# Optimization experiments

Hardware: AMD Instinct MI355X
Metric: run time of the kernel (lower is better)

## Reference

```python
import jax, jax.numpy as jnp
import numpy as np

DN = ('NHWC', 'HWIO', 'NHWC')

def conv(x, w, stride=1):
    return jax.lax.conv_general_dilated(x, w, (stride, stride), 'SAME', dimension_numbers=DN)

def up2(x):
    return jnp.repeat(jnp.repeat(x, 2, axis=1), 2, axis=2)

def nms(boxes, scores, max_output=100, iou_thresh=0.5):
    # greedy sequential NMS, fixed trip count, padded outputs
    NEG = jnp.float32(-1e30)
    area = (boxes[:, 2] - boxes[:, 0]) * (boxes[:, 3] - boxes[:, 1])  # [N]
    def step(sw, _):
        idx = jnp.argmax(sw)
        s = sw[idx]
        b = boxes[idx]
        valid = s > NEG * 0.5
        y1 = jnp.maximum(b[0], boxes[:, 0]); x1 = jnp.maximum(b[1], boxes[:, 1])
        y2 = jnp.minimum(b[2], boxes[:, 2]); x2 = jnp.minimum(b[3], boxes[:, 3])
        inter = jnp.maximum(y2 - y1, 0.0) * jnp.maximum(x2 - x1, 0.0)
        barea = (b[2] - b[0]) * (b[3] - b[1])
        iou = inter / (barea + area - inter + 1e-9)
        sw = jnp.where(iou > iou_thresh, NEG, sw)  # suppress (includes self)
        out_b = jnp.where(valid, b, jnp.zeros(4, boxes.dtype))
        out_s = jnp.where(valid, s, jnp.float32(0.0))
        return sw, (out_b, out_s)
    _, (sel_boxes, sel_scores) = jax.lax.scan(step, scores, None, length=max_output)
    return sel_boxes, sel_scores

def setup_inputs() -> dict:
    key = jax.random.key(0)
    ks = jax.random.split(key, 16)
    def w(k, shape):
        fan_in = shape[0] * shape[1] * shape[2]
        return jax.random.normal(k, shape, jnp.float32) * jnp.sqrt(2.0 / fan_in)
    return {
        'inputs': jax.random.normal(ks[0], (1, 512, 512, 3), jnp.float32),
        # backbone (resnet50-style channel widths, strides 2/4/8/16/32)
        'w_stem': w(ks[1], (7, 7, 3, 64)),
        'w_c2': w(ks[2], (3, 3, 64, 256)),
        'w_c3': w(ks[3], (3, 3, 256, 512)),
        'w_c4': w(ks[4], (3, 3, 512, 1024)),
        'w_c5': w(ks[5], (3, 3, 1024, 2048)),
        # FPN laterals + output convs (channels=256)
        'l3': w(ks[6], (1, 1, 512, 256)),
        'l4': w(ks[7], (1, 1, 1024, 256)),
        'l5': w(ks[8], (1, 1, 2048, 256)),
        'o3': w(ks[9], (3, 3, 256, 256)),
        'o4': w(ks[10], (3, 3, 256, 256)),
        'o5': w(ks[11], (3, 3, 256, 256)),
        # RPN: shared 3x3 + obj head (num_anchors=1) + bbox head (4*num_anchors)
        'w_rpn': w(ks[12], (3, 3, 256, 256)),
        'w_obj': w(ks[13], (1, 1, 256, 1)),
        'w_box': w(ks[14], (1, 1, 256, 4)),
    }

def reference(inputs, w_stem, w_c2, w_c3, w_c4, w_c5, l3, l4, l5, o3, o4, o5, w_rpn, w_obj, w_box):
    relu = jax.nn.relu
    # backbone
    s = relu(conv(inputs, w_stem, 2))   # 256x256x64
    c2 = relu(conv(s, w_c2, 2))         # 128x128x256
    c3 = relu(conv(c2, w_c3, 2))        # 64x64x512
    c4 = relu(conv(c3, w_c4, 2))        # 32x32x1024
    c5 = relu(conv(c4, w_c5, 2))        # 16x16x2048
    # FPN
    p5 = conv(c5, l5)
    p4 = conv(c4, l4) + up2(p5)
    p3 = conv(c3, l3) + up2(p4)
    p3, p4, p5 = conv(p3, o3), conv(p4, o4), conv(p5, o5)
    # RPN over all levels (bbox deltas computed per original but unused downstream)
    obj_logits = []
    for p in (p3, p4, p5):
        t = relu(conv(p, w_rpn))
        obj_logits.append(conv(t, w_obj))
        _ = conv(t, w_box)
    obj = obj_logits[0]  # [B, h, w, A]
    B, h, w_, A = obj.shape
    scores = jax.nn.sigmoid(obj).reshape(B, -1)  # [B, h*w*A]
    # anchor grid (fixed 0.1-sized boxes), faithful to TF meshgrid default 'xy' indexing
    yy = jnp.linspace(0.0, 1.0, h)
    xx = jnp.linspace(0.0, 1.0, w_)
    Y, X = jnp.meshgrid(yy, xx)  # shape [w, h]
    boxes = jnp.stack([Y - 0.05, X - 0.05, Y + 0.05, X + 0.05], axis=-1)
    boxes = jnp.clip(boxes, 0.0, 1.0).reshape(-1, 4)  # [w*h, 4]
    sel_boxes, sel_scores = nms(boxes, scores[0], max_output=100, iou_thresh=0.5)
    return sel_boxes, sel_scores
```

## Files before the change

### kernel.cpp

```cpp
#include <hip/hip_runtime.h>
#include <hip/hip_bf16.h>

typedef float f4 __attribute__((ext_vector_type(4)));
typedef short s8v __attribute__((ext_vector_type(8)));
typedef unsigned short us4 __attribute__((ext_vector_type(4)));
typedef unsigned short us8 __attribute__((ext_vector_type(8)));

#define AP 40

__global__ __launch_bounds__(256) void stem_kernel(
    const float* __restrict__ in, const float* __restrict__ w,
    float* __restrict__ out)
{
  __shared__ float in_lds[37 * 37 * 3];
  __shared__ float w_lds[7 * 7 * 3 * 64];
  const int tid = threadIdx.x;
  const int ty0 = (blockIdx.x >> 4) * 16;
  const int tx0 = (blockIdx.x & 15) * 16;

  for (int idx = tid; idx < 9408; idx += 256) w_lds[idx] = w[idx];
  for (int idx = tid; idx < 4107; idx += 256) {
    int ci = idx % 3;
    int rem = idx / 3;
    int ix = rem % 37, iy = rem / 37;
    int gy = ty0 * 2 - 2 + iy, gx = tx0 * 2 - 2 + ix;
    float v = 0.f;
    if ((unsigned)gy < 512u && (unsigned)gx < 512u)
      v = in[(gy * 512 + gx) * 3 + ci];
    in_lds[idx] = v;
  }
  __syncthreads();

  const int co = (tid & 15) * 4;
  const int py = tid >> 4;
  f4 acc[16];
#pragma unroll
  for (int px = 0; px < 16; ++px) acc[px] = (f4)0.f;

  for (int ky = 0; ky < 7; ++ky)
    for (int kx = 0; kx < 7; ++kx)
#pragma unroll
      for (int ci = 0; ci < 3; ++ci) {
        f4 wv = *(const f4*)&w_lds[(((ky * 7 + kx) * 3) + ci) * 64 + co];
        const float* ip = &in_lds[((2 * py + ky) * 37 + kx) * 3 + ci];
#pragma unroll
        for (int px = 0; px < 16; ++px) {
          float iv = ip[px * 6];
          acc[px] += iv * wv;
        }
      }

#pragma unroll
  for (int px = 0; px < 16; ++px) {
    int oy = ty0 + py, ox = tx0 + px;
    f4 o = acc[px];
#pragma unroll
    for (int c = 0; c < 4; ++c) o[c] = fmaxf(o[c], 0.f);
    *(f4*)&out[(oy * 256 + ox) * 64 + co] = o;
  }
}

__global__ __launch_bounds__(256) void wsplit_kernel(
    const float* __restrict__ w, unsigned short* __restrict__ wt,
    int C_in, int C_out, int taps)
{
  __shared__ float t[64][68];
  const int tid = threadIdx.x;
  const int tap = blockIdx.z;
  const int ci0 = blockIdx.x * 64;
  const int co0 = blockIdx.y * 64;
  const size_t lstride = (size_t)taps * C_in * C_out;

#pragma unroll
  for (int q = 0; q < 4; ++q) {
    int f = q * 256 + tid;
    int r = f >> 4, c = f & 15;
    f4 v = *(const f4*)&w[((size_t)(tap * C_in + ci0 + r)) * C_out + co0 + c * 4];
    *(f4*)&t[r][c * 4] = v;
  }
  __syncthreads();

#pragma unroll
  for (int q = 0; q < 4; ++q) {
    int f = q * 256 + tid;
    int r = f >> 4, c = f & 15;
    us4 h, m, l;
#pragma unroll
    for (int u = 0; u < 4; ++u) {
      float s = t[c * 4 + u][r];
      unsigned int ub = __float_as_uint(s);
      unsigned short hh = (unsigned short)(ub >> 16);
      float r1 = s - __uint_as_float((unsigned int)hh << 16);
      unsigned short mm = (unsigned short)(__float_as_uint(r1) >> 16);
      float r2 = r1 - __uint_as_float((unsigned int)mm << 16);
      unsigned short ll = (unsigned short)(__float_as_uint(r2) >> 16);
      h[u] = hh; m[u] = mm; l[u] = ll;
    }
    size_t base = ((size_t)tap * C_out + co0 + r) * C_in + ci0 + c * 4;
    *(us4*)&wt[base] = h;
    *(us4*)&wt[lstride + base] = m;
    *(us4*)&wt[2 * lstride + base] = l;
  }
}

__global__ __launch_bounds__(256, 2) void conv_mfma(
    const float* __restrict__ in, const unsigned short* __restrict__ wt,
    float* __restrict__ pout,
    int H_in, int W_in, int C_in, int wshift, int C_out,
    int stride, int pad, int ci_per_z, int npix, int relu)
{
  __shared__ __align__(16) unsigned short At[3][128][AP];
  __shared__ __align__(16) unsigned short Bt[3][128][AP];
  const int tid = threadIdx.x;

  const int nwg = gridDim.x * gridDim.y * gridDim.z;
  const int hwid = blockIdx.x + gridDim.x * (blockIdx.y + gridDim.y * blockIdx.z);
  const int wid = ((nwg & 7) == 0) ? (hwid & 7) * (nwg >> 3) + (hwid >> 3) : hwid;
  const int bx = wid % gridDim.x;
  const int brem = wid / gridDim.x;
  const int by = brem % gridDim.y;
  const int bz = brem / gridDim.y;

  const int pix_base = bx * 128;
  const int co_base = by * 128;
  const int ci_z0 = bz * ci_per_z;
  const int wmask = (1 << wshift) - 1;
  const size_t lstride = (size_t)9 * C_in * C_out;

  const int lane = tid & 63, wv = tid >> 6;
  const int pixhalf = (wv >> 1) * 64, cohalf = (wv & 1) * 64;
  const int fm = lane & 15, fq = lane >> 4;

  int a_pix[4], a_c4[4], a_ys[4], a_xs[4];
#pragma unroll
  for (int q = 0; q < 4; ++q) {
    int f = q * 256 + tid;
    a_pix[q] = f >> 3; a_c4[q] = f & 7;
    int p = pix_base + a_pix[q];
    a_ys[q] = (p >> wshift) * stride - pad;
    a_xs[q] = (p & wmask) * stride - pad;
  }
  int b_col[2], b_seg[2];
#pragma unroll
  for (int q = 0; q < 2; ++q) {
    int f = q * 256 + tid;
    b_col[q] = f >> 2; b_seg[q] = (f & 3) * 8;
  }

  const int nc = ci_per_z >> 5;
  const int ncsh = nc >> 1;
  const int nchunks = 9 * nc;

  f4 areg[4];
  us8 breg[6];
  auto issue_loads = [&](int c) {
    int tap = c >> ncsh;
    int ci = ci_z0 + (c & (nc - 1)) * 32;
    int ky = tap / 3, kx = tap - ky * 3;
#pragma unroll
    for (int q = 0; q < 4; ++q) {
      int iy = a_ys[q] + ky, ix = a_xs[q] + kx;
      bool v = ((unsigned)iy < (unsigned)H_in) & ((unsigned)ix < (unsigned)W_in);
      const float* p = in + (size_t)(iy * W_in + ix) * C_in + ci + a_c4[q] * 4;
      areg[q] = v ? *(const f4*)p : (f4)0.f;
    }
    const unsigned short* bb =
        wt + (size_t)tap * C_out * C_in + (size_t)co_base * C_in + ci;
#pragma unroll
    for (int L = 0; L < 3; ++L)
#pragma unroll
      for (int q = 0; q < 2; ++q)
        breg[L * 2 + q] = *(const us8*)(bb + (size_t)L * lstride +
                                        (size_t)b_col[q] * C_in + b_seg[q]);
  };

  us4 ah[4], am[4], al[4];
  auto convert = [&]() {
#pragma unroll
    for (int q = 0; q < 4; ++q) {
      f4 s4 = areg[q];
      us4 h, m, l;
#pragma unroll
      for (int u = 0; u < 4; ++u) {
        float s = s4[u];
        unsigned int ub = __float_as_uint(s);
        unsigned short hh = (unsigned short)(ub >> 16);
        float r1 = s - __uint_as_float((unsigned int)hh << 16);
        unsigned short mm = (unsigned short)(__float_as_uint(r1) >> 16);
        float r2 = r1 - __uint_as_float((unsigned int)mm << 16);
        unsigned short ll = (unsigned short)(__float_as_uint(r2) >> 16);
        h[u] = hh; m[u] = mm; l[u] = ll;
      }
      ah[q] = h; am[q] = m; al[q] = l;
    }
  };

  f4 acc[4][4];
#pragma unroll
  for (int i = 0; i < 4; ++i)
#pragma unroll
    for (int j = 0; j < 4; ++j) acc[i][j] = (f4)0.f;

  issue_loads(0);
  convert();

  for (int c = 0; c < nchunks; ++c) {
    __syncthreads();
#pragma unroll
    for (int q = 0; q < 4; ++q) {
      *(us4*)&At[0][a_pix[q]][a_c4[q] * 4] = ah[q];
      *(us4*)&At[1][a_pix[q]][a_c4[q] * 4] = am[q];
      *(us4*)&At[2][a_pix[q]][a_c4[q] * 4] = al[q];
    }
#pragma unroll
    for (int L = 0; L < 3; ++L)
#pragma unroll
      for (int q = 0; q < 2; ++q)
        *(us8*)&Bt[L][b_col[q]][b_seg[q]] = breg[L * 2 + q];
    __syncthreads();

    const bool more = (c + 1 < nchunks);
    if (more) issue_loads(c + 1);

    s8v Bh[4], Bm[4], Bl[4];
#pragma unroll
    for (int j = 0; j < 4; ++j) {
      Bh[j] = *(const s8v*)&Bt[0][cohalf + j * 16 + fm][fq * 8];
      Bm[j] = *(const s8v*)&Bt[1][cohalf + j * 16 + fm][fq * 8];
      Bl[j] = *(const s8v*)&Bt[2][cohalf + j * 16 + fm][fq * 8];
    }
    {
      s8v Ah[4];
#pragma unroll
      for (int i = 0; i < 4; ++i)
        Ah[i] = *(const s8v*)&At[0][pixhalf + i * 16 + fm][fq * 8];
#pragma unroll
      for (int i = 0; i < 4; ++i)
#pragma unroll
        for (int j = 0; j < 4; ++j) {
          acc[i][j] = __builtin_amdgcn_mfma_f32_16x16x32_bf16(Ah[i], Bh[j], acc[i][j], 0, 0, 0);
          acc[i][j] = __builtin_amdgcn_mfma_f32_16x16x32_bf16(Ah[i], Bm[j], acc[i][j], 0, 0, 0);
          acc[i][j] = __builtin_amdgcn_mfma_f32_16x16x32_bf16(Ah[i], Bl[j], acc[i][j], 0, 0, 0);
        }
    }
    {
      s8v Am[4];
#pragma unroll
      for (int i = 0; i < 4; ++i)
        Am[i] = *(const s8v*)&At[1][pixhalf + i * 16 + fm][fq * 8];
#pragma unroll
      for (int i = 0; i < 4; ++i)
#pragma unroll
        for (int j = 0; j < 4; ++j) {
          acc[i][j] = __builtin_amdgcn_mfma_f32_16x16x32_bf16(Am[i], Bh[j], acc[i][j], 0, 0, 0);
          acc[i][j] = __builtin_amdgcn_mfma_f32_16x16x32_bf16(Am[i], Bm[j], acc[i][j], 0, 0, 0);
        }
    }
    {
      s8v Al[4];
#pragma unroll
      for (int i = 0; i < 4; ++i)
        Al[i] = *(const s8v*)&At[2][pixhalf + i * 16 + fm][fq * 8];
#pragma unroll
      for (int i = 0; i < 4; ++i)
#pragma unroll
        for (int j = 0; j < 4; ++j)
          acc[i][j] = __builtin_amdgcn_mfma_f32_16x16x32_bf16(Al[i], Bh[j], acc[i][j], 0, 0, 0);
    }

    if (more) convert();
  }

  float* dst = pout + (size_t)bz * npix * C_out;
#pragma unroll
  for (int i = 0; i < 4; ++i) {
#pragma unroll
    for (int j = 0; j < 4; ++j) {
#pragma unroll
      for (int r = 0; r < 4; ++r) {
        int p = pix_base + pixhalf + i * 16 + fq * 4 + r;
        int co = co_base + cohalf + j * 16 + fm;
        float v = acc[i][j][r];
        if (relu) v = fmaxf(v, 0.f);
        dst[(size_t)p * C_out + co] = v;
      }
    }
  }
}

__global__ __launch_bounds__(256) void reduce_relu_kernel(
    const float* __restrict__ p, float* __restrict__ out, int n4, int Z, int relu)
{
  int idx = blockIdx.x * 256 + threadIdx.x;
  if (idx >= n4) return;
  const f4* pv = (const f4*)p;
  f4 s = pv[idx];
  for (int z = 1; z < Z; ++z) s += pv[(size_t)z * n4 + idx];
  if (relu) {
#pragma unroll
    for (int c = 0; c < 4; ++c) s[c] = fmaxf(s[c], 0.f);
  }
  ((f4*)out)[idx] = s;
}

__global__ __launch_bounds__(256) void gemm64(
    const float* __restrict__ in, const float* __restrict__ w,
    float* __restrict__ pout, int C_in, int C_out, int ci_per_z, int npix)
{
  __shared__ __align__(16) float As2[32][68];
  __shared__ __align__(16) float Bs[32][64];
  const int tid = threadIdx.x;
  const int pix_base = blockIdx.x * 64;
  const int co_base = blockIdx.y * 64;
  const int ci_z0 = blockIdx.z * ci_per_z;
  const int tx = tid & 15, ty = tid >> 4;

  int ga_pix[2], ga_c4[2];
#pragma unroll
  for (int q = 0; q < 2; ++q) {
    int f = q * 256 + tid;
    ga_pix[q] = f >> 3; ga_c4[q] = f & 7;
  }
  int gb_row[2], gb_c4[2];
#pragma unroll
  for (int q = 0; q < 2; ++q) {
    int f = q * 256 + tid;
    gb_row[q] = f >> 4; gb_c4[q] = f & 15;
  }

  f4 acc[4];
#pragma unroll
  for (int i = 0; i < 4; ++i) acc[i] = (f4)0.f;

  for (int ci = ci_z0; ci < ci_z0 + ci_per_z; ci += 32) {
    __syncthreads();
#pragma unroll
    for (int q = 0; q < 2; ++q) {
      f4 av = *(const f4*)&in[(size_t)(pix_base + ga_pix[q]) * C_in + ci + ga_c4[q] * 4];
#pragma unroll
      for (int u = 0; u < 4; ++u) As2[ga_c4[q] * 4 + u][ga_pix[q]] = av[u];
    }
#pragma unroll
    for (int q = 0; q < 2; ++q) {
      *(f4*)&Bs[gb_row[q]][gb_c4[q] * 4] =
          *(const f4*)&w[(size_t)(ci + gb_row[q]) * C_out + co_base + gb_c4[q] * 4];
    }
    __syncthreads();
#pragma unroll
    for (int kk = 0; kk < 32; ++kk) {
      f4 a = *(const f4*)&As2[kk][ty * 4];
      f4 b = *(const f4*)&Bs[kk][tx * 4];
#pragma unroll
      for (int i = 0; i < 4; ++i) acc[i] += a[i] * b;
    }
  }

  float* dst = pout + (size_t)blockIdx.z * npix * C_out;
#pragma unroll
  for (int i = 0; i < 4; ++i)
    *(f4*)&dst[(size_t)(pix_base + ty * 4 + i) * C_out + co_base + tx * 4] = acc[i];
}

__global__ __launch_bounds__(256) void reduce_up2_kernel(
    const float* __restrict__ p, const float* __restrict__ res,
    float* __restrict__ out, int n4, int Z, int wshift)
{
  int idx = blockIdx.x * 256 + threadIdx.x;
  if (idx >= n4) return;
  const f4* pv = (const f4*)p;
  f4 s = pv[idx];
  for (int z = 1; z < Z; ++z) s += pv[(size_t)z * n4 + idx];
  if (res) {
    int pix = idx >> 6, c4 = idx & 63;
    int oy = pix >> wshift, ox = pix & ((1 << wshift) - 1);
    int rp = ((oy >> 1) << (wshift - 1)) + (ox >> 1);
    s += ((const f4*)res)[rp * 64 + c4];
  }
  ((f4*)out)[idx] = s;
}

__global__ __launch_bounds__(256) void obj_sigmoid_kernel(
    const float* __restrict__ t, const float* __restrict__ wobj,
    float* __restrict__ scores)
{
  __shared__ float wl[256];
  const int tid = threadIdx.x;
  wl[tid] = wobj[tid];
  __syncthreads();
  const int pix = blockIdx.x * 64 + (tid >> 2);
  const int c0 = (tid & 3) * 64;
  float acc = 0.f;
#pragma unroll
  for (int k = 0; k < 16; ++k) {
    f4 tv = *(const f4*)&t[(size_t)pix * 256 + c0 + k * 4];
    const float* wp = &wl[c0 + k * 4];
    acc += tv[0] * wp[0] + tv[1] * wp[1] + tv[2] * wp[2] + tv[3] * wp[3];
  }
  acc += __shfl_xor(acc, 1);
  acc += __shfl_xor(acc, 2);
  if ((tid & 3) == 0) scores[pix] = 1.f / (1.f + expf(-acc));
}

__global__ __launch_bounds__(1024) void nms_kernel(
    const float* __restrict__ scores, float* __restrict__ out)
{
  __shared__ unsigned long long keys[4096];
  __shared__ float acc_lds[100 * 8];
  __shared__ unsigned long long supm[16];
  __shared__ int n_sh;
  const int tid = threadIdx.x;
  const float inv63 = 1.0f / 63.0f;

  if (tid < 125) ((f4*)out)[tid] = (f4)0.f;

  unsigned long long kr[4];
  {
    f4 sv = ((const f4*)scores)[tid];
#pragma unroll
    for (int v = 0; v < 4; ++v) {
      unsigned int bits = __float_as_uint(sv[v]);
      kr[v] = ((unsigned long long)(0x40000000u - bits) << 16) |
              (unsigned long long)(tid * 4 + v);
    }
  }

#pragma unroll
  for (int kb = 1; kb <= 12; ++kb) {
    const int k = 1 << kb;
#pragma unroll
    for (int j = k >> 1; j >= 256; j >>= 1) {
      *(ulonglong2*)&keys[tid * 4] = ulonglong2{kr[0], kr[1]};
      *(ulonglong2*)&keys[tid * 4 + 2] = ulonglong2{kr[2], kr[3]};
      __syncthreads();
      ulonglong2 p0 = *(const ulonglong2*)&keys[(tid * 4) ^ j];
      ulonglong2 p1 = *(const ulonglong2*)&keys[((tid * 4) ^ j) + 2];
      unsigned long long pb[4] = {p0.x, p0.y, p1.x, p1.y};
#pragma unroll
      for (int v = 0; v < 4; ++v) {
        int e = tid * 4 + v;
        bool up = ((e & k) == 0);
        bool lower = ((e & j) == 0);
        bool keep_min = (lower == up);
        unsigned long long a = kr[v], b = pb[v];
        unsigned long long mn = a < b ? a : b;
        unsigned long long mx = a < b ? b : a;
        kr[v] = keep_min ? mn : mx;
      }
      __syncthreads();
    }
    {
      const int js = (k >> 1) < 128 ? (k >> 1) : 128;
#pragma unroll
      for (int j = js; j >= 4; j >>= 1) {
        const int lm = j >> 2;
        bool lower = ((tid & lm) == 0);
        bool up = ((tid & (k >> 2)) == 0);
        bool keep_min = (lower == up);
#pragma unroll
        for (int v = 0; v < 4; ++v) {
          unsigned long long b = __shfl_xor(kr[v], lm);
          unsigned long long a = kr[v];
          unsigned long long mn = a < b ? a : b;
          unsigned long long mx = a < b ? b : a;
          kr[v] = keep_min ? mn : mx;
        }
      }
    }
    if (k >= 4) {
#pragma unroll
      for (int v = 0; v < 2; ++v) {
        bool up = (((tid * 4 + v) & k) == 0);
        unsigned long long a = kr[v], b = kr[v + 2];
        if ((a > b) == up) { kr[v] = b; kr[v + 2] = a; }
      }
    }
    {
#pragma unroll
      for (int v = 0; v < 4; v += 2) {
        bool up = (((tid * 4 + v) & k) == 0);
        unsigned long long a = kr[v], b = kr[v + 1];
        if ((a > b) == up) { kr[v] = b; kr[v + 1] = a; }
      }
    }
  }

  *(ulonglong2*)&keys[tid * 4] = ulonglong2{kr[0], kr[1]};
  *(ulonglong2*)&keys[tid * 4 + 2] = ulonglong2{kr[2], kr[3]};
  if (tid == 0) n_sh = 0;
  __syncthreads();

  const int wv = tid >> 6, lane = tid & 63;
  int n = 0;
  for (int b = 0; b < 64 && n < 100; ++b) {
    unsigned long long kk = keys[b * 64 + lane];
    int idx = (int)(kk & 0xFFFF);
    int si = idx >> 6, sj = idx & 63;
    float y = sj * inv63, x = si * inv63;
    float c0 = fmaxf(y - 0.05f, 0.f), c1 = fmaxf(x - 0.05f, 0.f);
    float c2 = fminf(y + 0.05f, 1.f), c3 = fminf(x + 0.05f, 1.f);
    float carea = (c2 - c0) * (c3 - c1);

    bool sup = false;
    for (int a = wv; a < n; a += 16) {
      f4 ab = *(const f4*)&acc_lds[a * 8];
      float aarea = acc_lds[a * 8 + 4];
      float yy1 = fmaxf(ab[0], c0), xx1 = fmaxf(ab[1], c1);
      float yy2 = fminf(ab[2], c2), xx2 = fminf(ab[3], c3);
      float inter = fmaxf(yy2 - yy1, 0.f) * fmaxf(xx2 - xx1, 0.f);
      float iou = inter / (aarea + carea - inter + 1e-9f);
      sup = sup || (iou > 0.5f);
    }
    supm[wv] = __ballot(sup);
    __syncthreads();

    if (wv == 0) {
      unsigned long long ms = supm[0];
#pragma unroll
      for (int w = 1; w < 16; ++w) ms |= supm[w];
      bool sup0 = (ms >> lane) & 1ull;
      float sc = __uint_as_float(0x40000000u - (unsigned int)(kk >> 16));
      int nn = n;
      unsigned long long m = __ballot(!sup0);
      while (m != 0 && nn < 100) {
        int u = __builtin_ctzll(m);
        float b0 = __shfl(c0, u), b1 = __shfl(c1, u);
        float b2 = __shfl(c2, u), b3 = __shfl(c3, u);
        float ba = __shfl(carea, u);
        if (lane == u) {
          acc_lds[nn * 8 + 0] = c0; acc_lds[nn * 8 + 1] = c1;
          acc_lds[nn * 8 + 2] = c2; acc_lds[nn * 8 + 3] = c3;
          acc_lds[nn * 8 + 4] = carea;
          out[nn * 4 + 0] = c0; out[nn * 4 + 1] = c1;
          out[nn * 4 + 2] = c2; out[nn * 4 + 3] = c3;
          out[400 + nn] = sc;
          sup0 = true;
        }
        nn++;
        if (lane > u && !sup0) {
          float yy1 = fmaxf(b0, c0), xx1 = fmaxf(b1, c1);
          float yy2 = fminf(b2, c2), xx2 = fminf(b3, c3);
          float inter = fmaxf(yy2 - yy1, 0.f) * fmaxf(xx2 - xx1, 0.f);
          float iou = inter / (ba + carea - inter + 1e-9f);
          if (iou > 0.5f) sup0 = true;
        }
        m = __ballot(!sup0);
      }
      if (lane == 0) n_sh = nn;
    }
    __syncthreads();
    n = n_sh;
  }
}

extern "C" void kernel_launch(void* const* d_in, const int* in_sizes, int n_in,
                              void* d_out, int out_size, void* d_ws, size_t ws_size,
                              hipStream_t stream) {
  const float* x      = (const float*)d_in[0];
  const float* w_stem = (const float*)d_in[1];
  const float* w_c2   = (const float*)d_in[2];
  const float* w_c3   = (const float*)d_in[3];
  const float* w_c4   = (const float*)d_in[4];
  const float* w_c5   = (const float*)d_in[5];
  const float* l3     = (const float*)d_in[6];
  const float* l4     = (const float*)d_in[7];
  const float* l5     = (const float*)d_in[8];
  const float* o3w    = (const float*)d_in[9];
  const float* w_rpn  = (const float*)d_in[12];
  const float* w_obj  = (const float*)d_in[13];
  float* out = (float*)d_out;
  float* ws = (float*)d_ws;

  float* S   = ws;
  float* C2  = S   + 4194304;
  float* C3  = C2  + 4194304;
  float* C4  = C3  + 2097152;
  float* C5  = C4  + 1048576;
  float* P5  = C5  + 524288;
  float* P4  = P5  + 65536;
  float* P3P = P4  + 262144;
  float* P3  = P3P + 1048576;
  float* T   = P3  + 1048576;
  float* SC  = T   + 1048576;
  unsigned short* WT = (unsigned short*)(SC + 4096);
  float* PZ = (float*)(WT + 31457280);

  stem_kernel<<<256, 256, 0, stream>>>(x, w_stem, S);

  wsplit_kernel<<<dim3(1, 4, 9), 256, 0, stream>>>(w_c2, WT, 64, 256, 9);
  conv_mfma<<<dim3(128, 2, 2), 256, 0, stream>>>(
      S, WT, PZ, 256, 256, 64, 7, 256, 2, 0, 32, 16384, 0);
  reduce_relu_kernel<<<4096, 256, 0, stream>>>(PZ, C2, 1048576, 2, 1);

  wsplit_kernel<<<dim3(4, 8, 9), 256, 0, stream>>>(w_c3, WT, 256, 512, 9);
  conv_mfma<<<dim3(32, 4, 4), 256, 0, stream>>>(
      C2, WT, PZ, 128, 128, 256, 6, 512, 2, 0, 64, 4096, 0);
  reduce_relu_kernel<<<2048, 256, 0, stream>>>(PZ, C3, 524288, 4, 1);

  wsplit_kernel<<<dim3(8, 16, 9), 256, 0, stream>>>(w_c4, WT, 512, 1024, 9);
  conv_mfma<<<dim3(8, 8, 8), 256, 0, stream>>>(
      C3, WT, S, 64, 64, 512, 5, 1024, 2, 0, 64, 1024, 0);
  reduce_relu_kernel<<<1024, 256, 0, stream>>>(S, C4, 262144, 8, 1);

  wsplit_kernel<<<dim3(16, 32, 9), 256, 0, stream>>>(w_c5, WT, 1024, 2048, 9);
  conv_mfma<<<dim3(2, 16, 16), 256, 0, stream>>>(
      C4, WT, S, 32, 32, 1024, 4, 2048, 2, 0, 64, 256, 0);
  reduce_relu_kernel<<<512, 256, 0, stream>>>(S, C5, 131072, 16, 1);

  gemm64<<<dim3(4, 4, 8), 256, 0, stream>>>(C5, l5, S, 2048, 256, 256, 256);
  reduce_up2_kernel<<<64, 256, 0, stream>>>(S, nullptr, P5, 16384, 8, 4);
  gemm64<<<dim3(16, 4, 4), 256, 0, stream>>>(C4, l4, S, 1024, 256, 256, 1024);
  reduce_up2_kernel<<<256, 256, 0, stream>>>(S, P5, P4, 65536, 4, 5);
  gemm64<<<dim3(64, 4, 2), 256, 0, stream>>>(C3, l3, S, 512, 256, 256, 4096);
  reduce_up2_kernel<<<1024, 256, 0, stream>>>(S, P4, P3P, 262144, 2, 6);

  wsplit_kernel<<<dim3(4, 4, 9), 256, 0, stream>>>(o3w, WT, 256, 256, 9);
  conv_mfma<<<dim3(32, 2, 8), 256, 0, stream>>>(
      P3P, WT, S, 64, 64, 256, 6, 256, 1, 1, 32, 4096, 0);
  reduce_relu_kernel<<<1024, 256, 0, stream>>>(S, P3, 262144, 8, 0);

  wsplit_kernel<<<dim3(4, 4, 9), 256, 0, stream>>>(w_rpn, WT, 256, 256, 9);
  conv_mfma<<<dim3(32, 2, 8), 256, 0, stream>>>(
      P3, WT, S, 64, 64, 256, 6, 256, 1, 1, 32, 4096, 0);
  reduce_relu_kernel<<<1024, 256, 0, stream>>>(S, T, 262144, 8, 1);

  obj_sigmoid_kernel<<<64, 256, 0, stream>>>(T, w_obj, SC);
  nms_kernel<<<1, 1024, 0, stream>>>(SC, out);
}
```

Before: 619.9 us.

## Widen conv tiles to 256 output channels and fuse c2 split-K reduce into c3 loads

The implicit-GEMM conv kernel now runs 512 threads (8 waves) per block, with each block covering 256 output channels instead of 128, so every A tile is reused across twice as many channels. Grid y-dimensions are halved to match. The separate reduce+relu pass for c2 is removed: the c3 conv sums the two split-K partials and applies ReLU while loading its input (template ZIN/IRELU). This saves a kernel launch and a full write/read of C2, at the cost of reading both partials for every tap of the c3 conv, a larger LDS footprint and possibly lower occupancy.

```diff
diff --git a/kernel.cpp b/kernel.cpp
--- a/kernel.cpp
+++ b/kernel.cpp
@@ -103,14 +103,15 @@
   }
 }
 
-__global__ __launch_bounds__(256, 2) void conv_mfma(
+template <int ZIN, bool IRELU>
+__global__ __launch_bounds__(512, 2) void conv_mfma(
     const float* __restrict__ in, const unsigned short* __restrict__ wt,
     float* __restrict__ pout,
     int H_in, int W_in, int C_in, int wshift, int C_out,
-    int stride, int pad, int ci_per_z, int npix, int relu)
+    int stride, int pad, int ci_per_z, int npix, int relu, int zstride)
 {
   __shared__ __align__(16) unsigned short At[3][128][AP];
-  __shared__ __align__(16) unsigned short Bt[3][128][AP];
+  __shared__ __align__(16) unsigned short Bt[3][256][AP];
   const int tid = threadIdx.x;
 
   const int nwg = gridDim.x * gridDim.y * gridDim.z;
@@ -122,19 +123,20 @@
   const int bz = brem / gridDim.y;
 
   const int pix_base = bx * 128;
-  const int co_base = by * 128;
+  const int co_base = by * 256;
   const int ci_z0 = bz * ci_per_z;
   const int wmask = (1 << wshift) - 1;
   const size_t lstride = (size_t)9 * C_in * C_out;
 
   const int lane = tid & 63, wv = tid >> 6;
-  const int pixhalf = (wv >> 1) * 64, cohalf = (wv & 1) * 64;
+  const int pixhalf = (wv >> 2) * 64;
+  const int coq = (wv & 3) * 64;
   const int fm = lane & 15, fq = lane >> 4;
 
-  int a_pix[4], a_c4[4], a_ys[4], a_xs[4];
-#pragma unroll
-  for (int q = 0; q < 4; ++q) {
-    int f = q * 256 + tid;
+  int a_pix[2], a_c4[2], a_ys[2], a_xs[2];
+#pragma unroll
+  for (int q = 0; q < 2; ++q) {
+    int f = q * 512 + tid;
     a_pix[q] = f >> 3; a_c4[q] = f & 7;
     int p = pix_base + a_pix[q];
     a_ys[q] = (p >> wshift) * stride - pad;
@@ -143,7 +145,7 @@
   int b_col[2], b_seg[2];
 #pragma unroll
   for (int q = 0; q < 2; ++q) {
-    int f = q * 256 + tid;
+    int f = q * 512 + tid;
     b_col[q] = f >> 2; b_seg[q] = (f & 3) * 8;
   }
 
@@ -151,18 +153,27 @@
   const int ncsh = nc >> 1;
   const int nchunks = 9 * nc;
 
-  f4 areg[4];
-  us8 breg[6];
+  f4 areg[2];
+  us8 breg[3][2];
   auto issue_loads = [&](int c) {
     int tap = c >> ncsh;
     int ci = ci_z0 + (c & (nc - 1)) * 32;
     int ky = tap / 3, kx = tap - ky * 3;
 #pragma unroll
-    for (int q = 0; q < 4; ++q) {
+    for (int q = 0; q < 2; ++q) {
       int iy = a_ys[q] + ky, ix = a_xs[q] + kx;
       bool v = ((unsigned)iy < (unsigned)H_in) & ((unsigned)ix < (unsigned)W_in);
       const float* p = in + (size_t)(iy * W_in + ix) * C_in + ci + a_c4[q] * 4;
-      areg[q] = v ? *(const f4*)p : (f4)0.f;
+      f4 s = (f4)0.f;
+      if (v) {
+        s = *(const f4*)p;
+        if (ZIN > 1) {
+#pragma unroll
+          for (int z = 1; z < ZIN; ++z)
+            s += *(const f4*)(p + (size_t)z * zstride);
+        }
+      }
+      areg[q] = s;
     }
     const unsigned short* bb =
         wt + (size_t)tap * C_out * C_in + (size_t)co_base * C_in + ci;
@@ -170,15 +181,19 @@
     for (int L = 0; L < 3; ++L)
 #pragma unroll
       for (int q = 0; q < 2; ++q)
-        breg[L * 2 + q] = *(const us8*)(bb + (size_t)L * lstride +
-                                        (size_t)b_col[q] * C_in + b_seg[q]);
+        breg[L][q] = *(const us8*)(bb + (size_t)L * lstride +
+                                   (size_t)b_col[q] * C_in + b_seg[q]);
   };
 
-  us4 ah[4], am[4], al[4];
+  us4 ah[2], am[2], al[2];
   auto convert = [&]() {
 #pragma unroll
-    for (int q = 0; q < 4; ++q) {
+    for (int q = 0; q < 2; ++q) {
       f4 s4 = areg[q];
+      if (IRELU) {
+#pragma unroll
+        for (int u = 0; u < 4; ++u) s4[u] = fmaxf(s4[u], 0.f);
+      }
       us4 h, m, l;
 #pragma unroll
       for (int u = 0; u < 4; ++u) {
@@ -207,7 +222,7 @@
   for (int c = 0; c < nchunks; ++c) {
     __syncthreads();
 #pragma unroll
-    for (int q = 0; q < 4; ++q) {
+    for (int q = 0; q < 2; ++q) {
       *(us4*)&At[0][a_pix[q]][a_c4[q] * 4] = ah[q];
       *(us4*)&At[1][a_pix[q]][a_c4[q] * 4] = am[q];
       *(us4*)&At[2][a_pix[q]][a_c4[q] * 4] = al[q];
@@ -216,7 +231,7 @@
     for (int L = 0; L < 3; ++L)
 #pragma unroll
       for (int q = 0; q < 2; ++q)
-        *(us8*)&Bt[L][b_col[q]][b_seg[q]] = breg[L * 2 + q];
+        *(us8*)&Bt[L][b_col[q]][b_seg[q]] = breg[L][q];
     __syncthreads();
 
     const bool more = (c + 1 < nchunks);
@@ -225,9 +240,9 @@
     s8v Bh[4], Bm[4], Bl[4];
 #pragma unroll
     for (int j = 0; j < 4; ++j) {
-      Bh[j] = *(const s8v*)&Bt[0][cohalf + j * 16 + fm][fq * 8];
-      Bm[j] = *(const s8v*)&Bt[1][cohalf + j * 16 + fm][fq * 8];
-      Bl[j] = *(const s8v*)&Bt[2][cohalf + j * 16 + fm][fq * 8];
+      Bh[j] = *(const s8v*)&Bt[0][coq + j * 16 + fm][fq * 8];
+      Bm[j] = *(const s8v*)&Bt[1][coq + j * 16 + fm][fq * 8];
+      Bl[j] = *(const s8v*)&Bt[2][coq + j * 16 + fm][fq * 8];
     }
     {
       s8v Ah[4];
@@ -279,7 +294,7 @@
 #pragma unroll
       for (int r = 0; r < 4; ++r) {
         int p = pix_base + pixhalf + i * 16 + fq * 4 + r;
-        int co = co_base + cohalf + j * 16 + fm;
+        int co = co_base + coq + j * 16 + fm;
         float v = acc[i][j][r];
         if (relu) v = fmaxf(v, 0.f);
         dst[(size_t)p * C_out + co] = v;
@@ -587,23 +602,22 @@
   stem_kernel<<<256, 256, 0, stream>>>(x, w_stem, S);
 
   wsplit_kernel<<<dim3(1, 4, 9), 256, 0, stream>>>(w_c2, WT, 64, 256, 9);
-  conv_mfma<<<dim3(128, 2, 2), 256, 0, stream>>>(
-      S, WT, PZ, 256, 256, 64, 7, 256, 2, 0, 32, 16384, 0);
-  reduce_relu_kernel<<<4096, 256, 0, stream>>>(PZ, C2, 1048576, 2, 1);
+  conv_mfma<1, false><<<dim3(128, 1, 2), 512, 0, stream>>>(
+      S, WT, PZ, 256, 256, 64, 7, 256, 2, 0, 32, 16384, 0, 0);
 
   wsplit_kernel<<<dim3(4, 8, 9), 256, 0, stream>>>(w_c3, WT, 256, 512, 9);
-  conv_mfma<<<dim3(32, 4, 4), 256, 0, stream>>>(
-      C2, WT, PZ, 128, 128, 256, 6, 512, 2, 0, 64, 4096, 0);
-  reduce_relu_kernel<<<2048, 256, 0, stream>>>(PZ, C3, 524288, 4, 1);
+  conv_mfma<2, true><<<dim3(32, 2, 4), 512, 0, stream>>>(
+      PZ, WT, ws, 128, 128, 256, 6, 512, 2, 0, 64, 4096, 0, 4194304);
+  reduce_relu_kernel<<<2048, 256, 0, stream>>>(ws, C3, 524288, 4, 1);
 
   wsplit_kernel<<<dim3(8, 16, 9), 256, 0, stream>>>(w_c4, WT, 512, 1024, 9);
-  conv_mfma<<<dim3(8, 8, 8), 256, 0, stream>>>(
-      C3, WT, S, 64, 64, 512, 5, 1024, 2, 0, 64, 1024, 0);
+  conv_mfma<1, false><<<dim3(8, 4, 8), 512, 0, stream>>>(
+      C3, WT, S, 64, 64, 512, 5, 1024, 2, 0, 64, 1024, 0, 0);
   reduce_relu_kernel<<<1024, 256, 0, stream>>>(S, C4, 262144, 8, 1);
 
   wsplit_kernel<<<dim3(16, 32, 9), 256, 0, stream>>>(w_c5, WT, 1024, 2048, 9);
-  conv_mfma<<<dim3(2, 16, 16), 256, 0, stream>>>(
-      C4, WT, S, 32, 32, 1024, 4, 2048, 2, 0, 64, 256, 0);
+  conv_mfma<1, false><<<dim3(2, 8, 16), 512, 0, stream>>>(
+      C4, WT, S, 32, 32, 1024, 4, 2048, 2, 0, 64, 256, 0, 0);
   reduce_relu_kernel<<<512, 256, 0, stream>>>(S, C5, 131072, 16, 1);
 
   gemm64<<<dim3(4, 4, 8), 256, 0, stream>>>(C5, l5, S, 2048, 256, 256, 256);
@@ -614,13 +628,13 @@
   reduce_up2_kernel<<<1024, 256, 0, stream>>>(S, P4, P3P, 262144, 2, 6);
 
   wsplit_kernel<<<dim3(4, 4, 9), 256, 0, stream>>>(o3w, WT, 256, 256, 9);
-  conv_mfma<<<dim3(32, 2, 8), 256, 0, stream>>>(
-      P3P, WT, S, 64, 64, 256, 6, 256, 1, 1, 32, 4096, 0);
+  conv_mfma<1, false><<<dim3(32, 1, 8), 512, 0, stream>>>(
+      P3P, WT, S, 64, 64, 256, 6, 256, 1, 1, 32, 4096, 0, 0);
   reduce_relu_kernel<<<1024, 256, 0, stream>>>(S, P3, 262144, 8, 0);
 
   wsplit_kernel<<<dim3(4, 4, 9), 256, 0, stream>>>(w_rpn, WT, 256, 256, 9);
-  conv_mfma<<<dim3(32, 2, 8), 256, 0, stream>>>(
-      P3, WT, S, 64, 64, 256, 6, 256, 1, 1, 32, 4096, 0);
+  conv_mfma<1, false><<<dim3(32, 1, 8), 512, 0, stream>>>(
+      P3, WT, S, 64, 64, 256, 6, 256, 1, 1, 32, 4096, 0, 0);
   reduce_relu_kernel<<<1024, 256, 0, stream>>>(S, T, 262144, 8, 1);
 
   obj_sigmoid_kernel<<<64, 256, 0, stream>>>(T, w_obj, SC);
```

Result: slower. 636.9 us (+2.7%).
